# Optimization experiments

Hardware: AMD Instinct MI355X
Metric: run time of the kernel (lower is better)

## Reference

```python
import jax, jax.numpy as jnp
import numpy as np

D_PROJ = 256      # core d_proj
WIN = 1536        # win_small (mid path, L<=mid_thr)
STRIDE = 384      # stride_small


def setup_inputs() -> dict:
    key = jax.random.key(0)
    ks = jax.random.split(key, 6)
    B, L, d_h, T, d_g = 4, 8192, 1024, 512, 256
    H = jax.random.normal(ks[0], (B, L, d_h), jnp.float32)
    G = jax.random.normal(ks[1], (B, T, d_g), jnp.float32)
    attn_mask = jnp.ones((B, L), dtype=bool)
    Wq_core = jax.random.normal(ks[2], (d_g, D_PROJ), jnp.float32) / np.float32(np.sqrt(d_g))
    Wk_core = jax.random.normal(ks[3], (d_h, D_PROJ), jnp.float32) / np.float32(np.sqrt(d_h))
    Wq_win = jax.random.normal(ks[4], (d_g, d_h), jnp.float32) / np.float32(np.sqrt(d_g))
    Wk_win = jax.random.normal(ks[5], (d_h, d_h), jnp.float32) / np.float32(np.sqrt(d_h))
    return dict(H=H, G=G, attn_mask=attn_mask, Wq_core=Wq_core, Wk_core=Wk_core,
                Wq_win=Wq_win, Wk_win=Wk_win)


def _core_pool(Hk, G, mask, Wq_core, Wk_core):
    # GoSpecificWattiPooling: GO-query cross-attention pooling over residues.
    q = jnp.einsum('btg,gp->btp', G, Wq_core)                 # [B,T,P]
    k = jnp.einsum('bwd,dp->bwp', Hk, Wk_core)                # [B,W,P]
    scores = jnp.einsum('btp,bwp->btw', q, k) * (D_PROJ ** -0.5)
    scores = jnp.where(mask[:, None, :], scores, jnp.float32(-1e30))
    alpha = jax.nn.softmax(scores, axis=-1)                   # over residues
    return jnp.einsum('btw,bwd->btd', alpha, Hk)              # [B,T,d_h]


def _window_starts(L, win, stride):
    starts, s = [], 0
    while s < L:
        e = min(s + win, L)
        starts.append(s)
        if e == L:
            break
        s += stride
    return starts


def reference(H, G, attn_mask, Wq_core, Wk_core, Wq_win, Wk_win):
    B, L, D = H.shape
    T = G.shape[1]
    starts = jnp.asarray(_window_starts(L, WIN, STRIDE), jnp.int32)
    q_t = jnp.einsum('btg,gd->btd', G, Wq_win)                # [B,T,D]
    scale = D ** -0.5

    def step(carry, s0):
        m, ssum, z = carry
        Hk = jax.lax.dynamic_slice_in_dim(H, s0, WIN, axis=1)
        mk = jax.lax.dynamic_slice_in_dim(attn_mask, s0, WIN, axis=1)
        Zk = _core_pool(Hk, G, mk, Wq_core, Wk_core)          # [B,T,D]
        k_w = jnp.einsum('btd,de->bte', Zk, Wk_win)
        lw = (jnp.sum(q_t * k_w, axis=-1, keepdims=True) * scale).astype(jnp.float32)
        m_new = jnp.maximum(m, lw)
        exp_m = jnp.exp(m - m_new)
        exp_w = jnp.exp(lw - m_new)
        ssum = ssum * exp_m + exp_w
        z = z * exp_m + exp_w * Zk.astype(jnp.float32)
        return (m_new, ssum, z), None

    init = (jnp.full((B, T, 1), -jnp.inf, jnp.float32),
            jnp.zeros((B, T, 1), jnp.float32),
            jnp.zeros((B, T, D), jnp.float32))
    (m, ssum, z), _ = jax.lax.scan(step, init, starts)
    return (z / (ssum + 1e-8)).astype(H.dtype)
```

## Files before the change

### kernel.cpp

```cpp
#include <hip/hip_runtime.h>
#include <math.h>

constexpr int Bb = 4;
constexpr int Lb = 8192;
constexpr int Dh = 1024;
constexpr int Tt = 512;
constexpr int Dg = 256;
constexpr int Pp = 256;
constexpr int NW = 19;

typedef unsigned short u16;
typedef __bf16 bf16x8 __attribute__((ext_vector_type(8)));
typedef float f32x4 __attribute__((ext_vector_type(4)));

__device__ __forceinline__ u16 f2bf(float x) {
  union { float f; unsigned u; } v;
  v.f = x;
  unsigned r = v.u + 0x7FFFu + ((v.u >> 16) & 1u);
  return (u16)(r >> 16);
}
__device__ __forceinline__ float bf2f(unsigned v) {
  union { unsigned u; float f; } c;
  c.u = v << 16;
  return c.f;
}

#define GLDS16(g, l)                                                          \
  __builtin_amdgcn_global_load_lds(                                           \
      (const __attribute__((address_space(1))) void*)(g),                     \
      (__attribute__((address_space(3))) void*)(l), 16, 0, 0)

template <int OB, int ORD>
__global__ __launch_bounds__(256) void mgemm(const u16* __restrict__ A,
                                             const u16* __restrict__ B,
                                             void* __restrict__ C,
                                             int K, int lda, int ldb, int ldc,
                                             long long sA, long long sB,
                                             long long sC, long long sK,
                                             int kSplit, float alpha) {
  __shared__ u16 smem[8192];
  u16* As = smem;
  u16* Bs = smem + 4096;

  const int gx = gridDim.x, gy = gridDim.y;
  int flat = blockIdx.x + gx * (blockIdx.y + gy * blockIdx.z);
  const int nwg = gx * gy * (int)gridDim.z;
  const int q = nwg >> 3, r = nwg & 7;
  const int xcd = flat & 7, sub = flat >> 3;
  flat = (xcd < r ? xcd * (q + 1) : r * (q + 1) + (xcd - r) * q) + sub;
  int bmI, bnI, z;
  if (ORD == 0) {
    bmI = flat % gx;
    const int t = flat / gx;
    bnI = t % gy;
    z = t / gy;
  } else {
    bnI = flat % gy;
    const int t = flat / gy;
    bmI = t % gx;
    z = t / gx;
  }

  const int b = z / kSplit, ks = z % kSplit;
  const int kLen = K / kSplit;
  A += b * sA + (long long)ks * kLen;
  B += b * sB + (long long)ks * kLen;
  const long long cOff = (long long)b * sC + (long long)ks * sK;

  const int bm = bmI * 128;
  const int bn = bnI * 128;
  const int tid = threadIdx.x;
  const int l = tid & 63;
  const int wid = tid >> 6;
  const int wm = wid >> 1, wn = wid & 1;

  const int sr = l >> 2, sj = l & 3;
  const int skb = sj ^ ((sr >> 1) & 3);

  f32x4 acc[4][4];
#pragma unroll
  for (int i = 0; i < 4; i++)
#pragma unroll
    for (int j = 0; j < 4; j++) acc[i][j] = (f32x4){0.f, 0.f, 0.f, 0.f};

  const int rl = l & 15, kb = l >> 4;

  for (int k0 = 0; k0 < kLen; k0 += 32) {
    __syncthreads();
    {
      const int c1 = wid, c2 = wid + 4;
      GLDS16(A + (long long)(bm + c1 * 16 + sr) * lda + k0 + skb * 8,
             As + c1 * 512);
      GLDS16(A + (long long)(bm + c2 * 16 + sr) * lda + k0 + skb * 8,
             As + c2 * 512);
      GLDS16(B + (long long)(bn + c1 * 16 + sr) * ldb + k0 + skb * 8,
             Bs + c1 * 512);
      GLDS16(B + (long long)(bn + c2 * 16 + sr) * ldb + k0 + skb * 8,
             Bs + c2 * 512);
    }
    __syncthreads();

    bf16x8 af[4], bfr[4];
#pragma unroll
    for (int f = 0; f < 4; f++) {
      const int rowA = wm * 64 + f * 16 + rl;
      const int unitA = rowA * 4 + (kb ^ ((rowA >> 1) & 3));
      af[f] = *(const bf16x8*)(As + unitA * 8);
      const int rowB = wn * 64 + f * 16 + rl;
      const int unitB = rowB * 4 + (kb ^ ((rowB >> 1) & 3));
      bfr[f] = *(const bf16x8*)(Bs + unitB * 8);
    }
#pragma unroll
    for (int i = 0; i < 4; i++)
#pragma unroll
      for (int j = 0; j < 4; j++)
        acc[i][j] = __builtin_amdgcn_mfma_f32_16x16x32_bf16(af[i], bfr[j],
                                                            acc[i][j], 0, 0, 0);
  }

  float* Cf = (float*)C;
  u16* Cb = (u16*)C;
#pragma unroll
  for (int i = 0; i < 4; i++) {
    const int row0 = bm + wm * 64 + i * 16 + (l >> 4) * 4;
#pragma unroll
    for (int j = 0; j < 4; j++) {
      const int col = bn + wn * 64 + j * 16 + (l & 15);
#pragma unroll
      for (int r2 = 0; r2 < 4; r2++) {
        const float v = alpha * acc[i][j][r2];
        const long long idx = cOff + (long long)(row0 + r2) * ldc + col;
        if (OB)
          Cb[idx] = f2bf(v);
        else
          Cf[idx] = v;
      }
    }
  }
}

__global__ __launch_bounds__(256) void convk(const float* __restrict__ in,
                                             u16* __restrict__ out, long long n4) {
  for (long long i = (long long)blockIdx.x * 256 + threadIdx.x; i < n4;
       i += (long long)gridDim.x * 256) {
    const float4 v = ((const float4*)in)[i];
    ushort4 o;
    o.x = f2bf(v.x);
    o.y = f2bf(v.y);
    o.z = f2bf(v.z);
    o.w = f2bf(v.w);
    ((ushort4*)out)[i] = o;
  }
}

__global__ __launch_bounds__(256) void t32(const float* __restrict__ in,
                                           u16* __restrict__ out, int R, int C,
                                           long long sIn, long long sOut) {
  __shared__ float t[32][33];
  const int b = blockIdx.z;
  in += (long long)b * sIn;
  out += (long long)b * sOut;
  const int r0 = blockIdx.x * 32, c0 = blockIdx.y * 32;
  const int tx = threadIdx.x, ty = threadIdx.y;
#pragma unroll
  for (int i = 0; i < 4; i++)
    t[ty + i * 8][tx] = in[(long long)(r0 + ty + i * 8) * C + c0 + tx];
  __syncthreads();
#pragma unroll
  for (int i = 0; i < 4; i++)
    out[(long long)(c0 + ty + i * 8) * R + r0 + tx] = f2bf(t[tx][ty + i * 8]);
}

__global__ __launch_bounds__(256) void tb16(const u16* __restrict__ in,
                                            u16* __restrict__ out, int R, int C,
                                            long long sIn, long long sOut) {
  __shared__ u16 t[32][34];
  const int b = blockIdx.z;
  in += (long long)b * sIn;
  out += (long long)b * sOut;
  const int r0 = blockIdx.x * 32, c0 = blockIdx.y * 32;
  const int tx = threadIdx.x, ty = threadIdx.y;
#pragma unroll
  for (int i = 0; i < 4; i++)
    t[ty + i * 8][tx] = in[(long long)(r0 + ty + i * 8) * C + c0 + tx];
  __syncthreads();
#pragma unroll
  for (int i = 0; i < 4; i++)
    out[(long long)(c0 + ty + i * 8) * R + r0 + tx] = t[tx][ty + i * 8];
}

__global__ __launch_bounds__(256) void addout4(const float* __restrict__ p,
                                               float* __restrict__ out, long long n4) {
  for (long long i = (long long)blockIdx.x * 256 + threadIdx.x; i < n4;
       i += (long long)gridDim.x * 256) {
    const float4 a = ((const float4*)p)[i];
    const float4 b = ((const float4*)p)[i + n4];
    const float4 c = ((const float4*)p)[i + 2 * n4];
    const float4 d = ((const float4*)p)[i + 3 * n4];
    float4 o = make_float4((a.x + b.x) + (c.x + d.x), (a.y + b.y) + (c.y + d.y),
                           (a.z + b.z) + (c.z + d.z), (a.w + b.w) + (c.w + d.w));
    ((float4*)out)[i] = o;
  }
}

__global__ __launch_bounds__(256) void combine2(const float* __restrict__ S,
                                                const u16* __restrict__ V,
                                                u16* __restrict__ Gm) {
  __shared__ float Ss[Lb];
  __shared__ float mx_s[64], se_s[64], sv_s[64], coef_s[64];
  __shared__ float m_s[NW], cw_s[NW];

  const int bt = blockIdx.x;
  const float* Srow = S + (long long)bt * Lb;
  const u16* Vrow = V + (long long)bt * Lb;
  u16* Grow = Gm + (long long)bt * Lb;

  const int tid = threadIdx.x;
  const int ln = tid & 63;
  const int wid = tid >> 6;

  for (int i = tid; i < Lb / 4; i += 256) {
    const float4 v = ((const float4*)Srow)[i];
    *(float4*)&Ss[i * 4] = v;
  }
  __syncthreads();

  for (int i = 0; i < 16; i++) {
    const int c = wid * 16 + i;
    const int j0 = c * 128 + ln * 2;
    const float2 s2 = *(const float2*)&Ss[j0];
    float mx = fmaxf(s2.x, s2.y);
#pragma unroll
    for (int o = 32; o; o >>= 1) mx = fmaxf(mx, __shfl_xor(mx, o, 64));
    const unsigned vv = *(const unsigned*)(Vrow + j0);
    const float v0 = bf2f(vv & 0xffffu), v1 = bf2f(vv >> 16);
    const float e0 = __expf(s2.x - mx), e1 = __expf(s2.y - mx);
    float se = e0 + e1;
    float sv = e0 * v0 + e1 * v1;
#pragma unroll
    for (int o = 32; o; o >>= 1) {
      se += __shfl_xor(se, o, 64);
      sv += __shfl_xor(sv, o, 64);
    }
    if (ln == 0) {
      mx_s[c] = mx;
      se_s[c] = se;
      sv_s[c] = sv;
    }
  }
  __syncthreads();

  if (wid == 0) {
    float lw = -1e30f, mw = 0.f, dw = 1.f;
    if (ln < NW) {
      const int c0 = (ln == 18) ? 52 : 3 * ln;
      mw = -1e30f;
#pragma unroll
      for (int k = 0; k < 12; k++) mw = fmaxf(mw, mx_s[c0 + k]);
      float d = 0.f, n = 0.f;
#pragma unroll
      for (int k = 0; k < 12; k++) {
        const float r = __expf(mx_s[c0 + k] - mw);
        d = fmaf(se_s[c0 + k], r, d);
        n = fmaf(sv_s[c0 + k], r, n);
      }
      dw = d;
      lw = (n / d) * 0.03125f;
    }
    float M = lw;
#pragma unroll
    for (int o = 32; o; o >>= 1) M = fmaxf(M, __shfl_xor(M, o, 64));
    const float e = (ln < NW) ? __expf(lw - M) : 0.f;
    float ss = e;
#pragma unroll
    for (int o = 32; o; o >>= 1) ss += __shfl_xor(ss, o, 64);
    if (ln < NW) {
      m_s[ln] = mw;
      cw_s[ln] = e / (ss + 1e-8f) / dw;
    }
  }
  __syncthreads();

  if (tid < 64) {
    const int c = tid;
    const int wlo = (c <= 11) ? 0 : (c - 9) / 3;
    const int whi = min(17, c / 3);
    const float mx = mx_s[c];
    float cf = 0.f;
    for (int w = wlo; w <= whi; w++) cf = fmaf(cw_s[w], __expf(mx - m_s[w]), cf);
    if (c >= 52) cf = fmaf(cw_s[18], __expf(mx - m_s[18]), cf);
    coef_s[c] = cf;
  }
  __syncthreads();

  for (int l = tid; l < Lb; l += 256) {
    const int c = l >> 7;
    const float g = __expf(Ss[l] - mx_s[c]) * coef_s[c];
    Grow[l] = f2bf(g);
  }
}

extern "C" void kernel_launch(void* const* d_in, const int* in_sizes, int n_in,
                              void* d_out, int out_size, void* d_ws, size_t ws_size,
                              hipStream_t stream) {
  const float* H = (const float*)d_in[0];
  const float* G = (const float*)d_in[1];
  const float* Wq_core = (const float*)d_in[3];
  const float* Wk_core = (const float*)d_in[4];
  const float* Wq_win = (const float*)d_in[5];
  const float* Wk_win = (const float*)d_in[6];
  float* out = (float*)d_out;

  const size_t MB = (size_t)1 << 20;
  char* w = (char*)d_ws;
  u16* Hb    = (u16*)(w);
  u16* Vb    = (u16*)(w + 64 * MB);
  u16* HTb   = (u16*)(w + 64 * MB);
  float* S   = (float*)(w + 128 * MB);
  float* part = (float*)(w + 128 * MB);
  u16* Kfb   = (u16*)(w + 192 * MB);
  u16* qb    = (u16*)(w + 208 * MB);
  u16* qtb   = (u16*)(w + 209 * MB);
  u16* ub    = (u16*)(w + 213 * MB);
  u16* Wkwb  = (u16*)(w + 217 * MB);
  u16* WkcTb = (u16*)(w + 219 * MB);
  u16* WqcTb = (u16*)(w + 219 * MB + MB / 2);
  u16* WqwTb = (u16*)(w + 220 * MB);
  u16* Gb    = (u16*)(w + 221 * MB);
  u16* gb    = (u16*)(w + 192 * MB);

  convk<<<2048, 256, 0, stream>>>(H, Hb, (long long)Bb * Lb * Dh / 4);
  t32<<<dim3(32, 8, 1), dim3(32, 8), 0, stream>>>(Wk_core, WkcTb, Dh, Pp, 0, 0);
  t32<<<dim3(8, 8, 1), dim3(32, 8), 0, stream>>>(Wq_core, WqcTb, Dg, Pp, 0, 0);
  t32<<<dim3(8, 32, 1), dim3(32, 8), 0, stream>>>(Wq_win, WqwTb, Dg, Dh, 0, 0);
  convk<<<1024, 256, 0, stream>>>(Wk_win, Wkwb, (long long)Dh * Dh / 4);
  convk<<<512, 256, 0, stream>>>(G, Gb, (long long)Bb * Tt * Dg / 4);

  mgemm<1, 1><<<dim3(256, 2, 1), 256, 0, stream>>>(
      Hb, WkcTb, Kfb, Dh, Dh, Dh, Pp, 0, 0, 0, 0, 1, 1.f);

  mgemm<1, 0><<<dim3(16, 2, 1), 256, 0, stream>>>(
      Gb, WqcTb, qb, Dg, Dg, Dg, Pp, 0, 0, 0, 0, 1, 1.f);

  mgemm<1, 0><<<dim3(16, 8, 1), 256, 0, stream>>>(
      Gb, WqwTb, qtb, Dg, Dg, Dg, Dh, 0, 0, 0, 0, 1, 1.f);

  mgemm<1, 0><<<dim3(16, 8, 1), 256, 0, stream>>>(
      qtb, Wkwb, ub, Dh, Dh, Dh, Dh, 0, 0, 0, 0, 1, 1.f);

  mgemm<0, 0><<<dim3(4, 64, Bb), 256, 0, stream>>>(
      qb, Kfb, S, Pp, Pp, Pp, Lb, (long long)Tt * Pp, (long long)Lb * Pp,
      (long long)Tt * Lb, 0, 1, 0.0625f);

  mgemm<1, 0><<<dim3(4, 64, Bb), 256, 0, stream>>>(
      ub, Hb, Vb, Dh, Dh, Dh, Lb, (long long)Tt * Dh, (long long)Lb * Dh,
      (long long)Tt * Lb, 0, 1, 1.f);

  combine2<<<dim3(Bb * Tt), 256, 0, stream>>>(S, Vb, gb);

  tb16<<<dim3(Lb / 32, Dh / 32, Bb), dim3(32, 8), 0, stream>>>(
      Hb, HTb, Lb, Dh, (long long)Lb * Dh, (long long)Dh * Lb);

  mgemm<0, 0><<<dim3(4, 8, Bb * 4), 256, 0, stream>>>(
      gb, HTb, part, Lb, Lb, Lb, Dh, (long long)Tt * Lb, (long long)Dh * Lb,
      (long long)Tt * Dh, (long long)Bb * Tt * Dh, 4, 1.f);

  addout4<<<2048, 256, 0, stream>>>(part, out, (long long)Bb * Tt * Dh / 4);
}
```

Before: 329.5 us.

## Add 256x256 eight-wave GEMM, fuse H convert+transpose, split-K 8

```diff
diff --git a/kernel.cpp b/kernel.cpp
--- a/kernel.cpp
+++ b/kernel.cpp
@@ -29,6 +29,187 @@
   __builtin_amdgcn_global_load_lds(                                           \
       (const __attribute__((address_space(1))) void*)(g),                     \
       (__attribute__((address_space(3))) void*)(l), 16, 0, 0)
+
+__device__ __forceinline__ void stage_ops(const u16* __restrict__ A, int lda,
+                                          int bm, int kA, u16* As,
+                                          const u16* __restrict__ B, int ldb,
+                                          int bn, int kB, u16* Bs, int tid,
+                                          int wid) {
+  const int rr = tid >> 3;
+  const int c16 = (tid & 7) ^ (rr & 7);
+#pragma unroll
+  for (int cc = 0; cc < 4; cc++) {
+    const int r = cc * 64 + rr;
+    GLDS16(A + (long long)(bm + r) * lda + kA + c16 * 8,
+           As + cc * 4096 + wid * 512);
+  }
+#pragma unroll
+  for (int cc = 0; cc < 4; cc++) {
+    const int r = cc * 64 + rr;
+    GLDS16(B + (long long)(bn + r) * ldb + kB + c16 * 8,
+           Bs + cc * 4096 + wid * 512);
+  }
+}
+
+template <int OB>
+__global__ __launch_bounds__(512, 1) void gemm256(const u16* __restrict__ A,
+                                                  const u16* __restrict__ B,
+                                                  void* __restrict__ C,
+                                                  int K, int lda, int ldb,
+                                                  int ldc, long long sA,
+                                                  long long sB, long long sC,
+                                                  long long sK, int kSplit,
+                                                  float alpha) {
+  __shared__ u16 lds[65536];
+
+  const int gx = gridDim.x, gy = gridDim.y;
+  int flat = blockIdx.x + gx * (blockIdx.y + gy * blockIdx.z);
+  const int nwg = gx * gy * (int)gridDim.z;
+  const int q = nwg >> 3, r = nwg & 7;
+  const int xcd = flat & 7, sub = flat >> 3;
+  flat = (xcd < r ? xcd * (q + 1) : r * (q + 1) + (xcd - r) * q) + sub;
+  const int bmI = flat % gx;
+  const int t1 = flat / gx;
+  const int bnI = t1 % gy;
+  const int z = t1 / gy;
+
+  const int b = z / kSplit, ks = z % kSplit;
+  const int kLen = K / kSplit;
+  const int nt = kLen >> 6;
+  A += b * sA + (long long)ks * kLen;
+  B += b * sB + (long long)ks * kLen;
+  const long long cOff = (long long)b * sC + (long long)ks * sK;
+
+  const int bm = bmI * 256, bn = bnI * 256;
+  const int tid = threadIdx.x;
+  const int wid = tid >> 6, l = tid & 63;
+  const int wm = wid >> 2, wn = wid & 3;
+  const int rl = l & 15, kq = l >> 4;
+  const int xr = rl & 7;
+
+  f32x4 acc[8][4];
+#pragma unroll
+  for (int i = 0; i < 8; i++)
+#pragma unroll
+    for (int j = 0; j < 4; j++) acc[i][j] = (f32x4){0.f, 0.f, 0.f, 0.f};
+
+  stage_ops(A, lda, bm, 0, lds, B, ldb, bn, 0, lds + 32768, tid, wid);
+  stage_ops(A, lda, bm, 64, lds + 16384, B, ldb, bn, 64, lds + 49152, tid, wid);
+  asm volatile("s_waitcnt vmcnt(8)" ::: "memory");
+  __builtin_amdgcn_s_barrier();
+
+  for (int t = 0; t < nt; t++) {
+    const int cur = t & 1;
+    const u16* As = lds + cur * 16384;
+    const u16* Bs = lds + 32768 + cur * 16384;
+    bf16x8 a0[4][2], bb[4][2];
+
+#pragma unroll
+    for (int i = 0; i < 4; i++)
+#pragma unroll
+      for (int s = 0; s < 2; s++)
+        a0[i][s] = *(const bf16x8*)(As + (wm * 128 + i * 16 + rl) * 64 +
+                                    (((s * 4 + kq) ^ xr) << 3));
+#pragma unroll
+    for (int j = 0; j < 2; j++)
+#pragma unroll
+      for (int s = 0; s < 2; s++)
+        bb[j][s] = *(const bf16x8*)(Bs + (wn * 64 + j * 16 + rl) * 64 +
+                                    (((s * 4 + kq) ^ xr) << 3));
+    __builtin_amdgcn_s_barrier();
+    __builtin_amdgcn_s_setprio(1);
+#pragma unroll
+    for (int i = 0; i < 4; i++)
+#pragma unroll
+      for (int j = 0; j < 2; j++)
+#pragma unroll
+        for (int s = 0; s < 2; s++)
+          acc[i][j] = __builtin_amdgcn_mfma_f32_16x16x32_bf16(
+              a0[i][s], bb[j][s], acc[i][j], 0, 0, 0);
+    __builtin_amdgcn_s_setprio(0);
+    __builtin_amdgcn_s_barrier();
+
+#pragma unroll
+    for (int j = 2; j < 4; j++)
+#pragma unroll
+      for (int s = 0; s < 2; s++)
+        bb[j][s] = *(const bf16x8*)(Bs + (wn * 64 + j * 16 + rl) * 64 +
+                                    (((s * 4 + kq) ^ xr) << 3));
+    __builtin_amdgcn_s_barrier();
+    __builtin_amdgcn_s_setprio(1);
+#pragma unroll
+    for (int i = 0; i < 4; i++)
+#pragma unroll
+      for (int j = 2; j < 4; j++)
+#pragma unroll
+        for (int s = 0; s < 2; s++)
+          acc[i][j] = __builtin_amdgcn_mfma_f32_16x16x32_bf16(
+              a0[i][s], bb[j][s], acc[i][j], 0, 0, 0);
+    __builtin_amdgcn_s_setprio(0);
+    __builtin_amdgcn_s_barrier();
+
+#pragma unroll
+    for (int i = 0; i < 4; i++)
+#pragma unroll
+      for (int s = 0; s < 2; s++)
+        a0[i][s] = *(const bf16x8*)(As + (wm * 128 + 64 + i * 16 + rl) * 64 +
+                                    (((s * 4 + kq) ^ xr) << 3));
+    __builtin_amdgcn_s_barrier();
+    __builtin_amdgcn_s_setprio(1);
+#pragma unroll
+    for (int i = 0; i < 4; i++)
+#pragma unroll
+      for (int j = 2; j < 4; j++)
+#pragma unroll
+        for (int s = 0; s < 2; s++)
+          acc[i + 4][j] = __builtin_amdgcn_mfma_f32_16x16x32_bf16(
+              a0[i][s], bb[j][s], acc[i + 4][j], 0, 0, 0);
+    __builtin_amdgcn_s_setprio(0);
+    __builtin_amdgcn_s_barrier();
+
+    if (t + 2 < nt) {
+      u16* Asw = (u16*)lds + cur * 16384;
+      u16* Bsw = (u16*)lds + 32768 + cur * 16384;
+      stage_ops(A, lda, bm, (t + 2) * 64, Asw, B, ldb, bn, (t + 2) * 64, Bsw,
+                tid, wid);
+    }
+    __builtin_amdgcn_s_setprio(1);
+#pragma unroll
+    for (int i = 0; i < 4; i++)
+#pragma unroll
+      for (int j = 0; j < 2; j++)
+#pragma unroll
+        for (int s = 0; s < 2; s++)
+          acc[i + 4][j] = __builtin_amdgcn_mfma_f32_16x16x32_bf16(
+              a0[i][s], bb[j][s], acc[i + 4][j], 0, 0, 0);
+    __builtin_amdgcn_s_setprio(0);
+    if (t + 2 < nt)
+      asm volatile("s_waitcnt vmcnt(8)" ::: "memory");
+    else
+      asm volatile("s_waitcnt vmcnt(0)" ::: "memory");
+    __builtin_amdgcn_s_barrier();
+  }
+
+  float* Cf = (float*)C;
+  u16* Cb = (u16*)C;
+#pragma unroll
+  for (int i = 0; i < 8; i++) {
+    const int row0 = bm + wm * 128 + i * 16 + kq * 4;
+#pragma unroll
+    for (int j = 0; j < 4; j++) {
+      const int col = bn + wn * 64 + j * 16 + rl;
+#pragma unroll
+      for (int r2 = 0; r2 < 4; r2++) {
+        const float v = alpha * acc[i][j][r2];
+        const long long idx = cOff + (long long)(row0 + r2) * ldc + col;
+        if (OB)
+          Cb[idx] = f2bf(v);
+        else
+          Cf[idx] = v;
+      }
+    }
+  }
+}
 
 template <int OB, int ORD>
 __global__ __launch_bounds__(256) void mgemm(const u16* __restrict__ A,
@@ -153,6 +334,28 @@
   }
 }
 
+__global__ __launch_bounds__(256) void convT(const float* __restrict__ in,
+                                             u16* __restrict__ outR,
+                                             u16* __restrict__ outT) {
+  __shared__ float t[32][33];
+  const int b = blockIdx.z;
+  const float* ib = in + (long long)b * Lb * Dh;
+  u16* oR = outR + (long long)b * Lb * Dh;
+  u16* oT = outT + (long long)b * Dh * Lb;
+  const int r0 = blockIdx.x * 32, c0 = blockIdx.y * 32;
+  const int tx = threadIdx.x, ty = threadIdx.y;
+#pragma unroll
+  for (int i = 0; i < 4; i++) {
+    const float v = ib[(long long)(r0 + ty + i * 8) * Dh + c0 + tx];
+    t[ty + i * 8][tx] = v;
+    oR[(long long)(r0 + ty + i * 8) * Dh + c0 + tx] = f2bf(v);
+  }
+  __syncthreads();
+#pragma unroll
+  for (int i = 0; i < 4; i++)
+    oT[(long long)(c0 + ty + i * 8) * Lb + r0 + tx] = f2bf(t[tx][ty + i * 8]);
+}
+
 __global__ __launch_bounds__(256) void t32(const float* __restrict__ in,
                                            u16* __restrict__ out, int R, int C,
                                            long long sIn, long long sOut) {
@@ -171,35 +374,20 @@
     out[(long long)(c0 + ty + i * 8) * R + r0 + tx] = f2bf(t[tx][ty + i * 8]);
 }
 
-__global__ __launch_bounds__(256) void tb16(const u16* __restrict__ in,
-                                            u16* __restrict__ out, int R, int C,
-                                            long long sIn, long long sOut) {
-  __shared__ u16 t[32][34];
-  const int b = blockIdx.z;
-  in += (long long)b * sIn;
-  out += (long long)b * sOut;
-  const int r0 = blockIdx.x * 32, c0 = blockIdx.y * 32;
-  const int tx = threadIdx.x, ty = threadIdx.y;
-#pragma unroll
-  for (int i = 0; i < 4; i++)
-    t[ty + i * 8][tx] = in[(long long)(r0 + ty + i * 8) * C + c0 + tx];
-  __syncthreads();
-#pragma unroll
-  for (int i = 0; i < 4; i++)
-    out[(long long)(c0 + ty + i * 8) * R + r0 + tx] = t[tx][ty + i * 8];
-}
-
-__global__ __launch_bounds__(256) void addout4(const float* __restrict__ p,
+__global__ __launch_bounds__(256) void addout8(const float* __restrict__ p,
                                                float* __restrict__ out, long long n4) {
   for (long long i = (long long)blockIdx.x * 256 + threadIdx.x; i < n4;
        i += (long long)gridDim.x * 256) {
-    const float4 a = ((const float4*)p)[i];
-    const float4 b = ((const float4*)p)[i + n4];
-    const float4 c = ((const float4*)p)[i + 2 * n4];
-    const float4 d = ((const float4*)p)[i + 3 * n4];
-    float4 o = make_float4((a.x + b.x) + (c.x + d.x), (a.y + b.y) + (c.y + d.y),
-                           (a.z + b.z) + (c.z + d.z), (a.w + b.w) + (c.w + d.w));
-    ((float4*)out)[i] = o;
+    float4 s = ((const float4*)p)[i];
+#pragma unroll
+    for (int j = 1; j < 8; j++) {
+      const float4 v = ((const float4*)p)[i + (long long)j * n4];
+      s.x += v.x;
+      s.y += v.y;
+      s.z += v.z;
+      s.w += v.w;
+    }
+    ((float4*)out)[i] = s;
   }
 }
 
@@ -293,10 +481,10 @@
   }
   __syncthreads();
 
-  for (int l = tid; l < Lb; l += 256) {
-    const int c = l >> 7;
-    const float g = __expf(Ss[l] - mx_s[c]) * coef_s[c];
-    Grow[l] = f2bf(g);
+  for (int ll = tid; ll < Lb; ll += 256) {
+    const int c = ll >> 7;
+    const float g = __expf(Ss[ll] - mx_s[c]) * coef_s[c];
+    Grow[ll] = f2bf(g);
   }
 }
 
@@ -314,22 +502,22 @@
   const size_t MB = (size_t)1 << 20;
   char* w = (char*)d_ws;
   u16* Hb    = (u16*)(w);
-  u16* Vb    = (u16*)(w + 64 * MB);
+  u16* gb    = (u16*)(w);
   u16* HTb   = (u16*)(w + 64 * MB);
   float* S   = (float*)(w + 128 * MB);
   float* part = (float*)(w + 128 * MB);
   u16* Kfb   = (u16*)(w + 192 * MB);
+  u16* Vb    = (u16*)(w + 192 * MB);
   u16* qb    = (u16*)(w + 208 * MB);
   u16* qtb   = (u16*)(w + 209 * MB);
-  u16* ub    = (u16*)(w + 213 * MB);
-  u16* Wkwb  = (u16*)(w + 217 * MB);
-  u16* WkcTb = (u16*)(w + 219 * MB);
-  u16* WqcTb = (u16*)(w + 219 * MB + MB / 2);
-  u16* WqwTb = (u16*)(w + 220 * MB);
-  u16* Gb    = (u16*)(w + 221 * MB);
-  u16* gb    = (u16*)(w + 192 * MB);
-
-  convk<<<2048, 256, 0, stream>>>(H, Hb, (long long)Bb * Lb * Dh / 4);
+  u16* Wkwb  = (u16*)(w + 213 * MB);
+  u16* WkcTb = (u16*)(w + 215 * MB);
+  u16* WqcTb = (u16*)(w + 215 * MB + MB / 2);
+  u16* WqwTb = (u16*)(w + 216 * MB);
+  u16* Gb    = (u16*)(w + 217 * MB);
+  u16* ub    = (u16*)(w + 224 * MB);
+
+  convT<<<dim3(Lb / 32, Dh / 32, Bb), dim3(32, 8), 0, stream>>>(H, Hb, HTb);
   t32<<<dim3(32, 8, 1), dim3(32, 8), 0, stream>>>(Wk_core, WkcTb, Dh, Pp, 0, 0);
   t32<<<dim3(8, 8, 1), dim3(32, 8), 0, stream>>>(Wq_core, WqcTb, Dg, Pp, 0, 0);
   t32<<<dim3(8, 32, 1), dim3(32, 8), 0, stream>>>(Wq_win, WqwTb, Dg, Dh, 0, 0);
@@ -348,22 +536,19 @@
   mgemm<1, 0><<<dim3(16, 8, 1), 256, 0, stream>>>(
       qtb, Wkwb, ub, Dh, Dh, Dh, Dh, 0, 0, 0, 0, 1, 1.f);
 
-  mgemm<0, 0><<<dim3(4, 64, Bb), 256, 0, stream>>>(
+  gemm256<0><<<dim3(2, 32, Bb), 512, 0, stream>>>(
       qb, Kfb, S, Pp, Pp, Pp, Lb, (long long)Tt * Pp, (long long)Lb * Pp,
       (long long)Tt * Lb, 0, 1, 0.0625f);
 
-  mgemm<1, 0><<<dim3(4, 64, Bb), 256, 0, stream>>>(
+  gemm256<1><<<dim3(2, 32, Bb), 512, 0, stream>>>(
       ub, Hb, Vb, Dh, Dh, Dh, Lb, (long long)Tt * Dh, (long long)Lb * Dh,
       (long long)Tt * Lb, 0, 1, 1.f);
 
   combine2<<<dim3(Bb * Tt), 256, 0, stream>>>(S, Vb, gb);
 
-  tb16<<<dim3(Lb / 32, Dh / 32, Bb), dim3(32, 8), 0, stream>>>(
-      Hb, HTb, Lb, Dh, (long long)Lb * Dh, (long long)Dh * Lb);
-
-  mgemm<0, 0><<<dim3(4, 8, Bb * 4), 256, 0, stream>>>(
+  gemm256<0><<<dim3(2, 4, Bb * 8), 512, 0, stream>>>(
       gb, HTb, part, Lb, Lb, Lb, Dh, (long long)Tt * Lb, (long long)Dh * Lb,
-      (long long)Tt * Dh, (long long)Bb * Tt * Dh, 4, 1.f);
-
-  addout4<<<2048, 256, 0, stream>>>(part, out, (long long)Bb * Tt * Dh / 4);
-}
+      (long long)Tt * Dh, (long long)Bb * Tt * Dh, 8, 1.f);
+
+  addout8<<<2048, 256, 0, stream>>>(part, out, (long long)Bb * Tt * Dh / 4);
+}
```

Result: faster. 308.3 us (-6.4%).
